# Kernel optimization log

Measured on AMD Instinct MI355X. Metric: run time of the kernel, lower is better.

The kernel has to match this reference:

```python
import jax, jax.numpy as jnp
import numpy as np

GROUPSIZE = 128
IN_FEATURES = 4096
OUT_FEATURES = 11008
K_BLOCKS = IN_FEATURES // GROUPSIZE  # 32
M_TOKENS = 512


def setup_inputs() -> dict:
    key = jax.random.key(0)
    k1, k2, k3, k4 = jax.random.split(key, 4)
    x = jax.random.normal(k1, (M_TOKENS, IN_FEATURES), dtype=jnp.float32)
    # packed 4-bit weights: (N, K_blocks, groupsize/2) bytes, two nibbles per byte
    qweight = jax.random.randint(k2, (OUT_FEATURES, K_BLOCKS, GROUPSIZE // 2), 0, 256, dtype=jnp.int32)
    # flat per-(n, k_block) scales, size K_blocks * N
    scales = jax.random.uniform(k3, (K_BLOCKS * OUT_FEATURES,), dtype=jnp.float32) * 0.01 + 0.001
    # flat packed zero points, size K_blocks * N / 2 bytes
    qzeros = jax.random.randint(k4, (K_BLOCKS * OUT_FEATURES // 2,), 0, 256, dtype=jnp.int32)
    return {"x": x, "qweight": qweight, "scales": scales, "qzeros": qzeros}


def _dequantize_4bit(qweight, scales, qzeros):
    # qweight: (N, Kb, gs/2) int32 bytes -> unpack low nibble first, then high
    lo = qweight & 15
    hi = (qweight >> 4) & 15
    w_int = jnp.stack([lo, hi], axis=-1).reshape(OUT_FEATURES, K_BLOCKS, GROUPSIZE)
    # qzeros: flat bytes -> interleaved nibbles -> (N, Kb)
    z = jnp.stack([qzeros & 15, (qzeros >> 4) & 15], axis=-1).reshape(OUT_FEATURES, K_BLOCKS)
    s = scales.reshape(OUT_FEATURES, K_BLOCKS)
    # (q - z) * s, blockwise
    w = (w_int - z[:, :, None]).astype(s.dtype) * s[:, :, None]
    return w.reshape(OUT_FEATURES, IN_FEATURES)  # (N, K)


def reference(x, qweight, scales, qzeros):
    fp_weight = _dequantize_4bit(qweight, scales, qzeros)  # (N, K)
    return x @ fp_weight.T  # (M, N)
```

## Files before the change

### kernel.cpp

```cpp
#include <hip/hip_runtime.h>
#include <hip/hip_fp16.h>

#define M_TOK 512
#define N_OUT 11008
#define K_IN  4096
#define KB    32

typedef _Float16 f16x8 __attribute__((ext_vector_type(8)));
typedef _Float16 f16x2 __attribute__((ext_vector_type(2)));
typedef float    f32x4 __attribute__((ext_vector_type(4)));

__global__ __launch_bounds__(256) void cvt_x_kernel(const float* __restrict__ x,
                                                    _Float16* __restrict__ xh) {
    int i = (blockIdx.x * 256 + threadIdx.x) * 8;
    float4 a = *(const float4*)(x + i);
    float4 b = *(const float4*)(x + i + 4);
    f16x8 v;
    v[0] = (_Float16)a.x; v[1] = (_Float16)a.y; v[2] = (_Float16)a.z; v[3] = (_Float16)a.w;
    v[4] = (_Float16)b.x; v[5] = (_Float16)b.y; v[6] = (_Float16)b.z; v[7] = (_Float16)b.w;
    *(f16x8*)(xh + i) = v;
}

__device__ __forceinline__ void gload_lds16(const void* g, void* l) {
    __builtin_amdgcn_global_load_lds(
        (const __attribute__((address_space(1))) void*)g,
        (__attribute__((address_space(3))) void*)l,
        16, 0, 0);
}

__device__ __forceinline__ unsigned int dq_pair(int b, f16x2 fz2, f16x2 ss2) {
    unsigned int u = ((unsigned int)b & 15u) |
                     (((unsigned int)b << 12) & 0xF0000u) |
                     0x64006400u;
    f16x2 h = __builtin_bit_cast(f16x2, u);
    f16x2 w = (h - fz2) * ss2;
    return __builtin_bit_cast(unsigned int, w);
}

__global__ __launch_bounds__(256, 3)
void gemm_w4_kernel(const int* __restrict__ qw,
                    const float* __restrict__ scales,
                    const int* __restrict__ qz,
                    const _Float16* __restrict__ xh,
                    float* __restrict__ out) {
    __shared__ __align__(16) char As[128 * 128];
    __shared__ __align__(16) char Bs[128 * 128];

    const int tid  = threadIdx.x;
    const int lane = tid & 63;
    const int wid  = tid >> 6;
    const int wm   = wid >> 1;
    const int wn   = wid & 1;
    const int r16  = lane & 15;
    const int g4   = lane >> 4;

    const int n0 = blockIdx.x * 128;
    const int m0 = blockIdx.y * 128;

    const char* xbytes = (const char*)xh;
    const char* asrc[4];
#pragma unroll
    for (int i = 0; i < 4; ++i) {
        int row = (tid >> 3) + i * 32;
        int cb  = (tid & 7) * 16;
        int cbl = cb ^ ((row & 7) << 4);
        asrc[i] = xbytes + (size_t)(m0 + row) * (K_IN * 2) + cbl;
    }

    const int n_loc = tid >> 1;
    const int half  = tid & 1;
    const int n_g   = n0 + n_loc;
    const int4* qbase = (const int4*)qw + ((size_t)n_g * 512 + half * 4);
    const int fbase = n_g * KB;
    unsigned int waddr[4];
#pragma unroll
    for (int q4 = 0; q4 < 4; ++q4) {
        int kt2 = half * 64 + q4 * 16;
        waddr[q4] = n_loc * 128 + (kt2 ^ ((n_loc & 7) << 4));
    }

    f32x4 acc[4][4];
#pragma unroll
    for (int mi = 0; mi < 4; ++mi)
#pragma unroll
        for (int ni = 0; ni < 4; ++ni)
            acc[mi][ni] = (f32x4){0.f, 0.f, 0.f, 0.f};

#pragma unroll 2
    for (int it = 0; it < K_IN / 64; ++it) {
        int4 qv0 = qbase[it * 8 + 0];
        int4 qv1 = qbase[it * 8 + 1];
        int4 qv2 = qbase[it * 8 + 2];
        int4 qv3 = qbase[it * 8 + 3];

        const int kb = it >> 1;
        const int f  = fbase + kb;
        const float s  = scales[f];
        const int  zb  = qz[f >> 1];
        const int  z   = (zb >> ((f & 1) * 4)) & 15;
        const _Float16 sh = (_Float16)s;
        const _Float16 fzh = (_Float16)(float)(1024 + z);
        const f16x2 ss2 = (f16x2){sh, sh};
        const f16x2 fz2 = (f16x2){fzh, fzh};

        __syncthreads();

#pragma unroll
        for (int i = 0; i < 4; ++i)
            gload_lds16(asrc[i] + it * 128, As + (wid * 64 + i * 256) * 16);

        {
            uint4 w;
            w.x = dq_pair(qv0.x, fz2, ss2); w.y = dq_pair(qv0.y, fz2, ss2);
            w.z = dq_pair(qv0.z, fz2, ss2); w.w = dq_pair(qv0.w, fz2, ss2);
            *(uint4*)(Bs + waddr[0]) = w;
            w.x = dq_pair(qv1.x, fz2, ss2); w.y = dq_pair(qv1.y, fz2, ss2);
            w.z = dq_pair(qv1.z, fz2, ss2); w.w = dq_pair(qv1.w, fz2, ss2);
            *(uint4*)(Bs + waddr[1]) = w;
            w.x = dq_pair(qv2.x, fz2, ss2); w.y = dq_pair(qv2.y, fz2, ss2);
            w.z = dq_pair(qv2.z, fz2, ss2); w.w = dq_pair(qv2.w, fz2, ss2);
            *(uint4*)(Bs + waddr[2]) = w;
            w.x = dq_pair(qv3.x, fz2, ss2); w.y = dq_pair(qv3.y, fz2, ss2);
            w.z = dq_pair(qv3.z, fz2, ss2); w.w = dq_pair(qv3.w, fz2, ss2);
            *(uint4*)(Bs + waddr[3]) = w;
        }

        __syncthreads();

#pragma unroll
        for (int kh = 0; kh < 2; ++kh) {
            f16x8 af[4], bf[4];
#pragma unroll
            for (int mi = 0; mi < 4; ++mi) {
                int row = wm * 64 + mi * 16 + r16;
                int off = row * 128 + ((kh * 64 + g4 * 16) ^ ((row & 7) << 4));
                af[mi] = *(const f16x8*)(As + off);
            }
#pragma unroll
            for (int ni = 0; ni < 4; ++ni) {
                int row = wn * 64 + ni * 16 + r16;
                int off = row * 128 + ((kh * 64 + g4 * 16) ^ ((row & 7) << 4));
                bf[ni] = *(const f16x8*)(Bs + off);
            }
#pragma unroll
            for (int mi = 0; mi < 4; ++mi)
#pragma unroll
                for (int ni = 0; ni < 4; ++ni)
                    acc[mi][ni] = __builtin_amdgcn_mfma_f32_16x16x32_f16(
                        af[mi], bf[ni], acc[mi][ni], 0, 0, 0);
        }
    }

#pragma unroll
    for (int mi = 0; mi < 4; ++mi) {
#pragma unroll
        for (int ni = 0; ni < 4; ++ni) {
            const int col   = n0 + wn * 64 + ni * 16 + r16;
            const int rbase = m0 + wm * 64 + mi * 16 + g4 * 4;
            f32x4 v = acc[mi][ni];
#pragma unroll
            for (int r = 0; r < 4; ++r)
                out[(size_t)(rbase + r) * N_OUT + col] = v[r];
        }
    }
}

extern "C" void kernel_launch(void* const* d_in, const int* in_sizes, int n_in,
                              void* d_out, int out_size, void* d_ws, size_t ws_size,
                              hipStream_t stream) {
    const float* x  = (const float*)d_in[0];
    const int*   qw = (const int*)d_in[1];
    const float* sc = (const float*)d_in[2];
    const int*   qz = (const int*)d_in[3];
    _Float16*    xh = (_Float16*)d_ws;
    float*       out = (float*)d_out;

    cvt_x_kernel<<<dim3((M_TOK * K_IN) / (256 * 8)), 256, 0, stream>>>(x, xh);

    gemm_w4_kernel<<<dim3(N_OUT / 128, M_TOK / 128), 256, 0, stream>>>(qw, sc, qz, xh, out);
}
```

Measured before the change: 249.8 us.

## Split K four ways with atomic accumulation and XCD-aware block remapping

Splits the K dimension into four slices so the GEMM launches 1376 blocks instead of 344, giving more parallelism across the GPU's compute units. Partial results are combined with float atomic adds into an output that a merged prep kernel zeroes first. The prep kernel also still converts x to fp16. A block index remap groups blocks by hardware XCD to improve cache locality, and the occupancy hint rises to 5 blocks per SM. The cost is extra output traffic from atomics and a zeroing pass, and the summation order becomes nondeterministic.

```diff
diff --git a/kernel.cpp b/kernel.cpp
--- a/kernel.cpp
+++ b/kernel.cpp
@@ -5,20 +5,29 @@
 #define N_OUT 11008
 #define K_IN  4096
 #define KB    32
+#define SPLITK 4
+#define NIT   (K_IN / SPLITK / 64)
 
 typedef _Float16 f16x8 __attribute__((ext_vector_type(8)));
 typedef _Float16 f16x2 __attribute__((ext_vector_type(2)));
 typedef float    f32x4 __attribute__((ext_vector_type(4)));
 
-__global__ __launch_bounds__(256) void cvt_x_kernel(const float* __restrict__ x,
-                                                    _Float16* __restrict__ xh) {
-    int i = (blockIdx.x * 256 + threadIdx.x) * 8;
-    float4 a = *(const float4*)(x + i);
-    float4 b = *(const float4*)(x + i + 4);
-    f16x8 v;
-    v[0] = (_Float16)a.x; v[1] = (_Float16)a.y; v[2] = (_Float16)a.z; v[3] = (_Float16)a.w;
-    v[4] = (_Float16)b.x; v[5] = (_Float16)b.y; v[6] = (_Float16)b.z; v[7] = (_Float16)b.w;
-    *(f16x8*)(xh + i) = v;
+__global__ __launch_bounds__(256) void prep_kernel(const float* __restrict__ x,
+                                                   _Float16* __restrict__ xh,
+                                                   float4* __restrict__ outz) {
+    int bid = blockIdx.x;
+    if (bid < 1024) {
+        int i = (bid * 256 + threadIdx.x) * 8;
+        float4 a = *(const float4*)(x + i);
+        float4 b = *(const float4*)(x + i + 4);
+        f16x8 v;
+        v[0] = (_Float16)a.x; v[1] = (_Float16)a.y; v[2] = (_Float16)a.z; v[3] = (_Float16)a.w;
+        v[4] = (_Float16)b.x; v[5] = (_Float16)b.y; v[6] = (_Float16)b.z; v[7] = (_Float16)b.w;
+        *(f16x8*)(xh + i) = v;
+    } else {
+        int i = (bid - 1024) * 256 + threadIdx.x;
+        outz[i] = make_float4(0.f, 0.f, 0.f, 0.f);
+    }
 }
 
 __device__ __forceinline__ void gload_lds16(const void* g, void* l) {
@@ -37,7 +46,7 @@
     return __builtin_bit_cast(unsigned int, w);
 }
 
-__global__ __launch_bounds__(256, 3)
+__global__ __launch_bounds__(256, 5)
 void gemm_w4_kernel(const int* __restrict__ qw,
                     const float* __restrict__ scales,
                     const int* __restrict__ qz,
@@ -45,6 +54,16 @@
                     float* __restrict__ out) {
     __shared__ __align__(16) char As[128 * 128];
     __shared__ __align__(16) char Bs[128 * 128];
+
+    const int hw  = blockIdx.x;
+    const int logical = (hw & 7) * 172 + (hw >> 3);
+    const int mx = logical & 3;
+    const int rest = logical >> 2;
+    const int ny = rest % 86;
+    const int kz = rest / 86;
+
+    const int n0 = ny * 128;
+    const int m0 = mx * 128;
 
     const int tid  = threadIdx.x;
     const int lane = tid & 63;
@@ -54,9 +73,6 @@
     const int r16  = lane & 15;
     const int g4   = lane >> 4;
 
-    const int n0 = blockIdx.x * 128;
-    const int m0 = blockIdx.y * 128;
-
     const char* xbytes = (const char*)xh;
     const char* asrc[4];
 #pragma unroll
@@ -64,14 +80,14 @@
         int row = (tid >> 3) + i * 32;
         int cb  = (tid & 7) * 16;
         int cbl = cb ^ ((row & 7) << 4);
-        asrc[i] = xbytes + (size_t)(m0 + row) * (K_IN * 2) + cbl;
+        asrc[i] = xbytes + (size_t)(m0 + row) * (K_IN * 2) + kz * 2048 + cbl;
     }
 
     const int n_loc = tid >> 1;
     const int half  = tid & 1;
     const int n_g   = n0 + n_loc;
-    const int4* qbase = (const int4*)qw + ((size_t)n_g * 512 + half * 4);
-    const int fbase = n_g * KB;
+    const int4* qbase = (const int4*)qw + ((size_t)n_g * 512 + kz * 128 + half * 4);
+    const int fbase = n_g * KB + kz * 8;
     unsigned int waddr[4];
 #pragma unroll
     for (int q4 = 0; q4 < 4; ++q4) {
@@ -87,14 +103,13 @@
             acc[mi][ni] = (f32x4){0.f, 0.f, 0.f, 0.f};
 
 #pragma unroll 2
-    for (int it = 0; it < K_IN / 64; ++it) {
+    for (int it = 0; it < NIT; ++it) {
         int4 qv0 = qbase[it * 8 + 0];
         int4 qv1 = qbase[it * 8 + 1];
         int4 qv2 = qbase[it * 8 + 2];
         int4 qv3 = qbase[it * 8 + 3];
 
-        const int kb = it >> 1;
-        const int f  = fbase + kb;
+        const int f  = fbase + (it >> 1);
         const float s  = scales[f];
         const int  zb  = qz[f >> 1];
         const int  z   = (zb >> ((f & 1) * 4)) & 15;
@@ -160,7 +175,7 @@
             f32x4 v = acc[mi][ni];
 #pragma unroll
             for (int r = 0; r < 4; ++r)
-                out[(size_t)(rbase + r) * N_OUT + col] = v[r];
+                unsafeAtomicAdd(&out[(size_t)(rbase + r) * N_OUT + col], v[r]);
         }
     }
 }
@@ -175,7 +190,7 @@
     _Float16*    xh = (_Float16*)d_ws;
     float*       out = (float*)d_out;
 
-    cvt_x_kernel<<<dim3((M_TOK * K_IN) / (256 * 8)), 256, 0, stream>>>(x, xh);
+    prep_kernel<<<dim3(1024 + 5504), 256, 0, stream>>>(x, xh, (float4*)out);
 
-    gemm_w4_kernel<<<dim3(N_OUT / 128, M_TOK / 128), 256, 0, stream>>>(qw, sc, qz, xh, out);
+    gemm_w4_kernel<<<dim3(1376), 256, 0, stream>>>(qw, sc, qz, xh, out);
 }
```

New measurement: 415.8 us. +66.5%, slower.

## Halve N tile to 64 and remap blocks across XCDs for L2 locality

Applied to the files above, without the earlier changes.

Shrinks the output tile from 128x128 to 128x64, giving 688 workgroups instead of 344, and raises the occupancy hint to 4 blocks per CU. A swizzled 1D block index spreads consecutive logical tiles across the 8 XCDs so that the four M-tiles sharing the same weight columns land on the same XCD. This improves wave count and load balance across CUs and lets dequantized weights be reused within one L2. The cost is more reloading of x tiles per output and a lower MFMA-to-load ratio per block.

```diff
diff --git a/kernel.cpp b/kernel.cpp
--- a/kernel.cpp
+++ b/kernel.cpp
@@ -37,14 +37,22 @@
     return __builtin_bit_cast(unsigned int, w);
 }
 
-__global__ __launch_bounds__(256, 3)
+__global__ __launch_bounds__(256, 4)
 void gemm_w4_kernel(const int* __restrict__ qw,
                     const float* __restrict__ scales,
                     const int* __restrict__ qz,
                     const _Float16* __restrict__ xh,
                     float* __restrict__ out) {
     __shared__ __align__(16) char As[128 * 128];
-    __shared__ __align__(16) char Bs[128 * 128];
+    __shared__ __align__(16) char Bs[64 * 128];
+
+    const int hw  = blockIdx.x;
+    const int logical = (hw & 7) * 86 + (hw >> 3);
+    const int mx = logical & 3;
+    const int ny = logical >> 2;
+
+    const int n0 = ny * 64;
+    const int m0 = mx * 128;
 
     const int tid  = threadIdx.x;
     const int lane = tid & 63;
@@ -53,9 +61,6 @@
     const int wn   = wid & 1;
     const int r16  = lane & 15;
     const int g4   = lane >> 4;
-
-    const int n0 = blockIdx.x * 128;
-    const int m0 = blockIdx.y * 128;
 
     const char* xbytes = (const char*)xh;
     const char* asrc[4];
@@ -67,34 +72,31 @@
         asrc[i] = xbytes + (size_t)(m0 + row) * (K_IN * 2) + cbl;
     }
 
-    const int n_loc = tid >> 1;
-    const int half  = tid & 1;
+    const int n_loc = tid >> 2;
+    const int q     = tid & 3;
     const int n_g   = n0 + n_loc;
-    const int4* qbase = (const int4*)qw + ((size_t)n_g * 512 + half * 4);
+    const int4* qbase = (const int4*)qw + ((size_t)n_g * 512 + q * 2);
     const int fbase = n_g * KB;
-    unsigned int waddr[4];
+    unsigned int waddr[2];
 #pragma unroll
-    for (int q4 = 0; q4 < 4; ++q4) {
-        int kt2 = half * 64 + q4 * 16;
-        waddr[q4] = n_loc * 128 + (kt2 ^ ((n_loc & 7) << 4));
+    for (int j = 0; j < 2; ++j) {
+        int kt2 = q * 32 + j * 16;
+        waddr[j] = n_loc * 128 + (kt2 ^ ((n_loc & 7) << 4));
     }
 
-    f32x4 acc[4][4];
+    f32x4 acc[4][2];
 #pragma unroll
     for (int mi = 0; mi < 4; ++mi)
 #pragma unroll
-        for (int ni = 0; ni < 4; ++ni)
+        for (int ni = 0; ni < 2; ++ni)
             acc[mi][ni] = (f32x4){0.f, 0.f, 0.f, 0.f};
 
 #pragma unroll 2
     for (int it = 0; it < K_IN / 64; ++it) {
         int4 qv0 = qbase[it * 8 + 0];
         int4 qv1 = qbase[it * 8 + 1];
-        int4 qv2 = qbase[it * 8 + 2];
-        int4 qv3 = qbase[it * 8 + 3];
 
-        const int kb = it >> 1;
-        const int f  = fbase + kb;
+        const int f  = fbase + (it >> 1);
         const float s  = scales[f];
         const int  zb  = qz[f >> 1];
         const int  z   = (zb >> ((f & 1) * 4)) & 15;
@@ -117,19 +119,13 @@
             w.x = dq_pair(qv1.x, fz2, ss2); w.y = dq_pair(qv1.y, fz2, ss2);
             w.z = dq_pair(qv1.z, fz2, ss2); w.w = dq_pair(qv1.w, fz2, ss2);
             *(uint4*)(Bs + waddr[1]) = w;
-            w.x = dq_pair(qv2.x, fz2, ss2); w.y = dq_pair(qv2.y, fz2, ss2);
-            w.z = dq_pair(qv2.z, fz2, ss2); w.w = dq_pair(qv2.w, fz2, ss2);
-            *(uint4*)(Bs + waddr[2]) = w;
-            w.x = dq_pair(qv3.x, fz2, ss2); w.y = dq_pair(qv3.y, fz2, ss2);
-            w.z = dq_pair(qv3.z, fz2, ss2); w.w = dq_pair(qv3.w, fz2, ss2);
-            *(uint4*)(Bs + waddr[3]) = w;
         }
 
         __syncthreads();
 
 #pragma unroll
         for (int kh = 0; kh < 2; ++kh) {
-            f16x8 af[4], bf[4];
+            f16x8 af[4], bf[2];
 #pragma unroll
             for (int mi = 0; mi < 4; ++mi) {
                 int row = wm * 64 + mi * 16 + r16;
@@ -137,15 +133,15 @@
                 af[mi] = *(const f16x8*)(As + off);
             }
 #pragma unroll
-            for (int ni = 0; ni < 4; ++ni) {
-                int row = wn * 64 + ni * 16 + r16;
+            for (int ni = 0; ni < 2; ++ni) {
+                int row = wn * 32 + ni * 16 + r16;
                 int off = row * 128 + ((kh * 64 + g4 * 16) ^ ((row & 7) << 4));
                 bf[ni] = *(const f16x8*)(Bs + off);
             }
 #pragma unroll
             for (int mi = 0; mi < 4; ++mi)
 #pragma unroll
-                for (int ni = 0; ni < 4; ++ni)
+                for (int ni = 0; ni < 2; ++ni)
                     acc[mi][ni] = __builtin_amdgcn_mfma_f32_16x16x32_f16(
                         af[mi], bf[ni], acc[mi][ni], 0, 0, 0);
         }
@@ -154,8 +150,8 @@
 #pragma unroll
     for (int mi = 0; mi < 4; ++mi) {
 #pragma unroll
-        for (int ni = 0; ni < 4; ++ni) {
-            const int col   = n0 + wn * 64 + ni * 16 + r16;
+        for (int ni = 0; ni < 2; ++ni) {
+            const int col   = n0 + wn * 32 + ni * 16 + r16;
             const int rbase = m0 + wm * 64 + mi * 16 + g4 * 4;
             f32x4 v = acc[mi][ni];
 #pragma unroll
@@ -177,5 +173,5 @@
 
     cvt_x_kernel<<<dim3((M_TOK * K_IN) / (256 * 8)), 256, 0, stream>>>(x, xh);
 
-    gemm_w4_kernel<<<dim3(N_OUT / 128, M_TOK / 128), 256, 0, stream>>>(qw, sc, qz, xh, out);
+    gemm_w4_kernel<<<dim3(688), 256, 0, stream>>>(qw, sc, qz, xh, out);
 }
```

After: 233.8 us. 1.07x faster.
